# Kernel optimization log

Hardware: AMD Instinct MI355X
Metric: run time of the kernel (lower is better)

## Reference

```python
import jax, jax.numpy as jnp
import numpy as np

N = 100000
E = 1600000
D_IN = 256
D_OUT = 128
ALPHA = 0.2  # LeakyReLU negative slope


def setup_inputs() -> dict:
    key = jax.random.key(0)
    k1, k2, k3, k4, k5 = jax.random.split(key, 5)
    x = jax.random.normal(k1, (N, D_IN), dtype=jnp.float32)
    # random edges + self-loops so every destination row has >=1 incoming edge
    src = jax.random.randint(k2, (E - N,), 0, N)
    dst = jax.random.randint(k3, (E - N,), 0, N)
    loops = jnp.arange(N)
    edge = jnp.stack([jnp.concatenate([src, loops]),
                      jnp.concatenate([dst, loops])]).astype(jnp.int64)  # [2, E]
    W = jax.random.normal(k4, (D_IN, D_OUT), dtype=jnp.float32) * 0.1
    a = jax.random.normal(k5, (1, 2 * D_OUT), dtype=jnp.float32) * 0.1
    return {"x": x, "edge": edge, "W": W, "a": a}


def reference(x, edge, W, a):
    n = x.shape[0]
    d_out = W.shape[1]
    h = x @ W  # [n, d_out]
    src, dst = edge[0], edge[1]
    # a @ concat(h[src], h[dst]) decomposes into two per-node projections
    f_src = h @ a[0, :d_out]   # [n]
    f_dst = h @ a[0, d_out:]   # [n]
    tmp = f_src[src] + f_dst[dst]                      # [E]
    lrelu = jnp.where(tmp > 0, tmp, ALPHA * tmp)
    edge_e = jnp.exp(-lrelu)                           # [E]
    # spmm(A, ones) -> rowsum; spmm(A, h) -> weighted aggregation (rows = src)
    e_rowsum = jax.ops.segment_sum(edge_e, src, num_segments=n)           # [n]
    hh = jax.ops.segment_sum(edge_e[:, None] * h[dst], src, num_segments=n)  # [n, d_out]
    hh = hh / e_rowsum[:, None]
    return jax.nn.elu(hh)  # end=False -> apply ELU
```

## Files before the change

kernel.cpp:

```cpp
#include <hip/hip_runtime.h>

#define D_IN 256
#define D_OUT 128
#define ALPHA 0.2f
#define RB 64
#define RBSH 6
#define NBMAX 1600
#define CH 8192
#define CAPG 1536
#define OVFCAP 32768
#define LDA 264

typedef __attribute__((ext_vector_type(8))) short bf16x8;
typedef __attribute__((ext_vector_type(4))) float f32x4;

__device__ inline unsigned short f2bf(float f) {
    unsigned int u = __float_as_uint(f);
    return (unsigned short)((u + 0x7FFFu + ((u >> 16) & 1u)) >> 16);
}
__device__ inline float bf2f(unsigned short u) {
    return __uint_as_float(((unsigned int)u) << 16);
}

__global__ __launch_bounds__(256) void k_wt(const float* __restrict__ W,
                                            unsigned short* __restrict__ WTb) {
    const int ncol = blockIdx.x;
    const int k = threadIdx.x;
    WTb[(size_t)ncol * 256 + k] = f2bf(W[(size_t)k * 128 + ncol]);
}

__global__ __launch_bounds__(256, 4) void k_gemm(const float* __restrict__ x,
                                                 const unsigned short* __restrict__ WTb,
                                                 const float* __restrict__ a,
                                                 unsigned short* __restrict__ hb,
                                                 float* __restrict__ f_src,
                                                 float* __restrict__ f_dst, int n) {
    __shared__ unsigned short sA[64 * LDA];
    __shared__ float sFp[64][2][2];
    const int t = threadIdx.x;
    const int l = t & 63;
    const int w = t >> 6;
    const int wr = w >> 1, wc = w & 1;
    const int row0 = blockIdx.x * 64;
    const int col0 = wc * 64;
    const int lr = l & 15;
    const int g = l >> 4;
    const int lk8 = g * 8;

    {
        const int rr = t >> 5;
        const int cc = (t & 31) * 8;
        #pragma unroll
        for (int it = 0; it < 8; ++it) {
            int r = it * 8 + rr;
            int gr = row0 + r;
            float4 fa, fb;
            if (gr < n) {
                fa = *(const float4*)&x[(size_t)gr * D_IN + cc];
                fb = *(const float4*)&x[(size_t)gr * D_IN + cc + 4];
            } else {
                fa = make_float4(0.f, 0.f, 0.f, 0.f);
                fb = fa;
            }
            bf16x8 v;
            v[0] = (short)f2bf(fa.x); v[1] = (short)f2bf(fa.y);
            v[2] = (short)f2bf(fa.z); v[3] = (short)f2bf(fa.w);
            v[4] = (short)f2bf(fb.x); v[5] = (short)f2bf(fb.y);
            v[6] = (short)f2bf(fb.z); v[7] = (short)f2bf(fb.w);
            *(bf16x8*)&sA[r * LDA + cc] = v;
        }
    }
    __syncthreads();

    f32x4 acc[2][4] = {};
    const unsigned short* bp[4];
    #pragma unroll
    for (int ni = 0; ni < 4; ++ni)
        bp[ni] = WTb + (size_t)(col0 + ni * 16 + lr) * 256 + lk8;

    #pragma unroll
    for (int k0 = 0; k0 < D_IN; k0 += 32) {
        bf16x8 af[2], bfr[4];
        #pragma unroll
        for (int mi = 0; mi < 2; ++mi)
            af[mi] = *(const bf16x8*)&sA[(wr * 32 + mi * 16 + lr) * LDA + k0 + lk8];
        #pragma unroll
        for (int ni = 0; ni < 4; ++ni) bfr[ni] = *(const bf16x8*)(bp[ni] + k0);
        #pragma unroll
        for (int mi = 0; mi < 2; ++mi)
            #pragma unroll
            for (int ni = 0; ni < 4; ++ni)
                acc[mi][ni] = __builtin_amdgcn_mfma_f32_16x16x32_bf16(
                    af[mi], bfr[ni], acc[mi][ni], 0, 0, 0);
    }

    #pragma unroll
    for (int mi = 0; mi < 2; ++mi) {
        #pragma unroll
        for (int q = 0; q < 4; ++q) {
            int r = row0 + wr * 32 + mi * 16 + g * 4 + q;
            if (r < n) {
                #pragma unroll
                for (int ni = 0; ni < 4; ++ni)
                    hb[(size_t)r * D_OUT + col0 + ni * 16 + lr] =
                        f2bf(acc[mi][ni][q]);
            }
        }
    }

    float asv[4], adv[4];
    #pragma unroll
    for (int ni = 0; ni < 4; ++ni) {
        asv[ni] = a[col0 + ni * 16 + lr];
        adv[ni] = a[D_OUT + col0 + ni * 16 + lr];
    }
    #pragma unroll
    for (int mi = 0; mi < 2; ++mi) {
        #pragma unroll
        for (int q = 0; q < 4; ++q) {
            float fs = 0.f, fd = 0.f;
            #pragma unroll
            for (int ni = 0; ni < 4; ++ni) {
                float v = acc[mi][ni][q];
                fs = fmaf(v, asv[ni], fs);
                fd = fmaf(v, adv[ni], fd);
            }
            #pragma unroll
            for (int m = 1; m < 16; m <<= 1) {
                fs += __shfl_xor(fs, m);
                fd += __shfl_xor(fd, m);
            }
            if (lr == 0) {
                int rl = wr * 32 + mi * 16 + g * 4 + q;
                sFp[rl][wc][0] = fs;
                sFp[rl][wc][1] = fd;
            }
        }
    }
    __syncthreads();
    if (t < 64) {
        int r = row0 + t;
        if (r < n) {
            f_src[r] = sFp[t][0][0] + sFp[t][1][0];
            f_dst[r] = sFp[t][0][1] + sFp[t][1][1];
        }
    }
}

__global__ __launch_bounds__(256) void k_bfill(const int* __restrict__ src,
                                               const int* __restrict__ dst,
                                               int* __restrict__ gcnt,
                                               int2* __restrict__ ovf,
                                               int* __restrict__ gkeys, int E, int nb) {
    __shared__ int cnt[NBMAX];
    __shared__ int bas[NBMAX];
    const int t = threadIdx.x;
    const int e0 = blockIdx.x * CH;
    const int e1 = min(e0 + CH, E);
    for (int i = t; i < nb; i += 256) cnt[i] = 0;
    __syncthreads();
    for (int e = e0 + t; e < e1; e += 256) atomicAdd(&cnt[src[e] >> RBSH], 1);
    __syncthreads();
    for (int b = t; b < nb; b += 256) {
        int c = cnt[b];
        bas[b] = c ? atomicAdd(&gcnt[b], c) : 0;
        cnt[b] = 0;
    }
    __syncthreads();
    for (int e = e0 + t; e < e1; e += 256) {
        int s = src[e], d = dst[e];
        int b = s >> RBSH;
        int key = ((s & (RB - 1)) << 17) | d;
        int r = bas[b] + atomicAdd(&cnt[b], 1);
        if (r < CAPG) {
            gkeys[b * CAPG + r] = key;
        } else {
            int o = atomicAdd(&gcnt[nb], 1);
            if (o < OVFCAP) ovf[o] = make_int2(b, key);
        }
    }
}

__global__ __launch_bounds__(512, 8) void k_bagg(const unsigned short* __restrict__ hb,
                                                 const float* __restrict__ f_src,
                                                 const float* __restrict__ f_dst,
                                                 const int* __restrict__ gcnt,
                                                 const int2* __restrict__ ovf,
                                                 const int* __restrict__ gkeys,
                                                 float* __restrict__ out, int n, int nb) {
    __shared__ int2 sdw[CAPG];
    __shared__ int nbase[RB];
    __shared__ int ncnt[RB];
    __shared__ int ncur[RB];
    __shared__ float fsl[RB];
    __shared__ int sc[RB];
    const int t = threadIdx.x;
    const int b = blockIdx.x;
    const int s0 = b * RB;
    const int nn = min(RB, n - s0);
    const int beg = b * CAPG;
    const int stored = min(gcnt[b], CAPG);
    const int ovf_n = min(gcnt[nb], OVFCAP);

    for (int i = t; i < RB; i += 512) {
        ncnt[i] = 0;
        fsl[i] = (i < nn) ? f_src[s0 + i] : 0.f;
    }
    __syncthreads();

    for (int i = t; i < stored; i += 512)
        atomicAdd(&ncnt[gkeys[beg + i] >> 17], 1);
    __syncthreads();

    if (t < RB) sc[t] = ncnt[t];
    __syncthreads();
    for (int off = 1; off < RB; off <<= 1) {
        int v = 0;
        if (t < RB && t >= off) v = sc[t - off];
        __syncthreads();
        if (t < RB) sc[t] += v;
        __syncthreads();
    }
    if (t < RB) {
        nbase[t] = sc[t] - ncnt[t];
        ncur[t]  = sc[t] - ncnt[t];
    }
    __syncthreads();

    for (int i = t; i < stored; i += 512) {
        int k = gkeys[beg + i];
        int d = k & 0x1FFFF, ls = k >> 17;
        float tmp = fsl[ls] + f_dst[d];
        float w = __expf(-((tmp > 0.f) ? tmp : ALPHA * tmp));
        int pos = atomicAdd(&ncur[ls], 1);
        sdw[pos] = make_int2(d, __float_as_int(w));
    }
    __syncthreads();

    const int lane = t & 63, wid = t >> 6;
    const int cl = (lane & 31) * 4;
    const bool isB = lane >= 32;
    for (int ni = wid; ni < nn; ni += 8) {
        const int jb = nbase[ni];
        const int cn = ncnt[ni];
        const int halfA = (cn + 1) >> 1;
        const int halfB = cn - halfA;
        const int lim = isB ? halfB : halfA;
        const int jbh = jb + (isB ? halfA : 0);
        float a0 = 0.f, a1 = 0.f, a2 = 0.f, a3 = 0.f, rowsum = 0.f;
        #pragma unroll 4
        for (int it = 0; it < halfA; ++it) {
            bool valid = it < lim;
            int2 dw = sdw[valid ? (jbh + it) : jb];
            float w = valid ? __int_as_float(dw.y) : 0.f;
            ushort4 hv = *(const ushort4*)&hb[(size_t)dw.x * D_OUT + cl];
            rowsum += w;
            a0 = fmaf(w, bf2f(hv.x), a0);
            a1 = fmaf(w, bf2f(hv.y), a1);
            a2 = fmaf(w, bf2f(hv.z), a2);
            a3 = fmaf(w, bf2f(hv.w), a3);
        }
        if (ovf_n > 0) {
            for (int o = 0; o < ovf_n; ++o) {
                int2 ov = ovf[o];
                if (ov.x == b && (ov.y >> 17) == ni && !isB) {
                    int d = ov.y & 0x1FFFF;
                    float tmp = fsl[ni] + f_dst[d];
                    float w = __expf(-((tmp > 0.f) ? tmp : ALPHA * tmp));
                    ushort4 hv = *(const ushort4*)&hb[(size_t)d * D_OUT + cl];
                    rowsum += w;
                    a0 = fmaf(w, bf2f(hv.x), a0);
                    a1 = fmaf(w, bf2f(hv.y), a1);
                    a2 = fmaf(w, bf2f(hv.z), a2);
                    a3 = fmaf(w, bf2f(hv.w), a3);
                }
            }
        }
        rowsum += __shfl_xor(rowsum, 32);
        a0 += __shfl_xor(a0, 32);
        a1 += __shfl_xor(a1, 32);
        a2 += __shfl_xor(a2, 32);
        a3 += __shfl_xor(a3, 32);
        if (!isB) {
            float inv = 1.f / rowsum;
            a0 *= inv; a1 *= inv; a2 *= inv; a3 *= inv;
            a0 = (a0 > 0.f) ? a0 : (__expf(a0) - 1.f);
            a1 = (a1 > 0.f) ? a1 : (__expf(a1) - 1.f);
            a2 = (a2 > 0.f) ? a2 : (__expf(a2) - 1.f);
            a3 = (a3 > 0.f) ? a3 : (__expf(a3) - 1.f);
            *(float4*)&out[(size_t)(s0 + ni) * D_OUT + cl] =
                make_float4(a0, a1, a2, a3);
        }
    }
}

extern "C" void kernel_launch(void* const* d_in, const int* in_sizes, int n_in,
                              void* d_out, int out_size, void* d_ws, size_t ws_size,
                              hipStream_t stream) {
    const float* x    = (const float*)d_in[0];
    const int*   edge = (const int*)d_in[1];
    const float* W    = (const float*)d_in[2];
    const float* a    = (const float*)d_in[3];
    float* out = (float*)d_out;

    const int n = in_sizes[0] / D_IN;
    const int E = in_sizes[1] / 2;
    const int* src = edge;
    const int* dst = edge + E;
    const int nb = (n + RB - 1) / RB;

    char* p = (char*)d_ws;
    unsigned short* hb  = (unsigned short*)p; p += (size_t)n * D_OUT * sizeof(unsigned short);
    unsigned short* WTb = (unsigned short*)p; p += (size_t)D_OUT * D_IN * sizeof(unsigned short);
    float* f_src = (float*)p;  p += (size_t)n * sizeof(float);
    float* f_dst = (float*)p;  p += (size_t)n * sizeof(float);
    int*  gcnt   = (int*)p;    p += (size_t)(nb + 1) * sizeof(int);
    int2* ovf    = (int2*)p;   p += (size_t)OVFCAP * sizeof(int2);
    int*  gkeys  = (int*)p;    p += (size_t)nb * CAPG * sizeof(int);

    const int gemm_blocks = (n + 63) / 64;

    k_wt<<<D_OUT, 256, 0, stream>>>(W, WTb);
    k_gemm<<<gemm_blocks, 256, 0, stream>>>(x, WTb, a, hb, f_src, f_dst, n);

    hipMemsetAsync(gcnt, 0, (size_t)(nb + 1) * sizeof(int), stream);
    k_bfill<<<(E + CH - 1) / CH, 256, 0, stream>>>(src, dst, gcnt, ovf, gkeys, E, nb);
    k_bagg<<<nb, 512, 0, stream>>>(hb, f_src, f_dst, gcnt, ovf, gkeys, out, n, nb);
}
```

Before: 158.0 us.

## Enlarge GEMM row tile to 128 with split-K staging and XOR-swizzled LDS

The GEMM kernel now processes 128 rows per block instead of 64, so each wave computes a 64x64 tile and reuses each loaded W fragment across twice as many MFMAs. The x tile is staged in two K halves of 128 so the LDS footprint stays bounded, and an XOR swizzle replaces the old padded stride to avoid bank conflicts. The cost is more accumulator registers, an extra pair of barriers per block, and half as many blocks, which may reduce occupancy. The explicit occupancy hint in the launch bounds is also dropped.

```diff
diff --git a/kernel.cpp b/kernel.cpp
--- a/kernel.cpp
+++ b/kernel.cpp
@@ -9,7 +9,7 @@
 #define CH 8192
 #define CAPG 1536
 #define OVFCAP 32768
-#define LDA 264
+#define LKH 128
 
 typedef __attribute__((ext_vector_type(8))) short bf16x8;
 typedef __attribute__((ext_vector_type(4))) float f32x4;
@@ -29,76 +29,86 @@
     WTb[(size_t)ncol * 256 + k] = f2bf(W[(size_t)k * 128 + ncol]);
 }
 
-__global__ __launch_bounds__(256, 4) void k_gemm(const float* __restrict__ x,
-                                                 const unsigned short* __restrict__ WTb,
-                                                 const float* __restrict__ a,
-                                                 unsigned short* __restrict__ hb,
-                                                 float* __restrict__ f_src,
-                                                 float* __restrict__ f_dst, int n) {
-    __shared__ unsigned short sA[64 * LDA];
-    __shared__ float sFp[64][2][2];
+__global__ __launch_bounds__(256) void k_gemm(const float* __restrict__ x,
+                                              const unsigned short* __restrict__ WTb,
+                                              const float* __restrict__ a,
+                                              unsigned short* __restrict__ hb,
+                                              float* __restrict__ f_src,
+                                              float* __restrict__ f_dst, int n) {
+    __shared__ unsigned short sA[128 * LKH];
+    __shared__ float sFp[128][2][2];
     const int t = threadIdx.x;
     const int l = t & 63;
     const int w = t >> 6;
     const int wr = w >> 1, wc = w & 1;
-    const int row0 = blockIdx.x * 64;
+    const int row0 = blockIdx.x * 128;
     const int col0 = wc * 64;
     const int lr = l & 15;
     const int g = l >> 4;
     const int lk8 = g * 8;
 
-    {
-        const int rr = t >> 5;
-        const int cc = (t & 31) * 8;
-        #pragma unroll
-        for (int it = 0; it < 8; ++it) {
-            int r = it * 8 + rr;
-            int gr = row0 + r;
-            float4 fa, fb;
-            if (gr < n) {
-                fa = *(const float4*)&x[(size_t)gr * D_IN + cc];
-                fb = *(const float4*)&x[(size_t)gr * D_IN + cc + 4];
-            } else {
-                fa = make_float4(0.f, 0.f, 0.f, 0.f);
-                fb = fa;
-            }
-            bf16x8 v;
-            v[0] = (short)f2bf(fa.x); v[1] = (short)f2bf(fa.y);
-            v[2] = (short)f2bf(fa.z); v[3] = (short)f2bf(fa.w);
-            v[4] = (short)f2bf(fb.x); v[5] = (short)f2bf(fb.y);
-            v[6] = (short)f2bf(fb.z); v[7] = (short)f2bf(fb.w);
-            *(bf16x8*)&sA[r * LDA + cc] = v;
-        }
-    }
-    __syncthreads();
-
-    f32x4 acc[2][4] = {};
+    f32x4 acc[4][4] = {};
     const unsigned short* bp[4];
     #pragma unroll
     for (int ni = 0; ni < 4; ++ni)
         bp[ni] = WTb + (size_t)(col0 + ni * 16 + lr) * 256 + lk8;
 
     #pragma unroll
-    for (int k0 = 0; k0 < D_IN; k0 += 32) {
-        bf16x8 af[2], bfr[4];
+    for (int half = 0; half < 2; ++half) {
+        {
+            const int rr = t >> 4;
+            const int cc = (t & 15) * 8;
+            #pragma unroll
+            for (int it = 0; it < 8; ++it) {
+                int r = it * 16 + rr;
+                int gr = row0 + r;
+                float4 fa, fb;
+                if (gr < n) {
+                    const float* xp = &x[(size_t)gr * D_IN + half * LKH + cc];
+                    fa = *(const float4*)xp;
+                    fb = *(const float4*)(xp + 4);
+                } else {
+                    fa = make_float4(0.f, 0.f, 0.f, 0.f);
+                    fb = fa;
+                }
+                bf16x8 v;
+                v[0] = (short)f2bf(fa.x); v[1] = (short)f2bf(fa.y);
+                v[2] = (short)f2bf(fa.z); v[3] = (short)f2bf(fa.w);
+                v[4] = (short)f2bf(fb.x); v[5] = (short)f2bf(fb.y);
+                v[6] = (short)f2bf(fb.z); v[7] = (short)f2bf(fb.w);
+                int js = (cc >> 3) ^ ((r & 7) << 1);
+                *(bf16x8*)&sA[r * LKH + js * 8] = v;
+            }
+        }
+        __syncthreads();
+
         #pragma unroll
-        for (int mi = 0; mi < 2; ++mi)
-            af[mi] = *(const bf16x8*)&sA[(wr * 32 + mi * 16 + lr) * LDA + k0 + lk8];
-        #pragma unroll
-        for (int ni = 0; ni < 4; ++ni) bfr[ni] = *(const bf16x8*)(bp[ni] + k0);
-        #pragma unroll
-        for (int mi = 0; mi < 2; ++mi)
+        for (int k0 = 0; k0 < LKH; k0 += 32) {
+            bf16x8 af[4], bfr[4];
+            #pragma unroll
+            for (int mi = 0; mi < 4; ++mi) {
+                int row_l = wr * 64 + mi * 16 + lr;
+                int js = ((k0 >> 3) + g) ^ ((row_l & 7) << 1);
+                af[mi] = *(const bf16x8*)&sA[row_l * LKH + js * 8];
+            }
             #pragma unroll
             for (int ni = 0; ni < 4; ++ni)
-                acc[mi][ni] = __builtin_amdgcn_mfma_f32_16x16x32_bf16(
-                    af[mi], bfr[ni], acc[mi][ni], 0, 0, 0);
-    }
-
-    #pragma unroll
-    for (int mi = 0; mi < 2; ++mi) {
+                bfr[ni] = *(const bf16x8*)(bp[ni] + half * LKH + k0);
+            #pragma unroll
+            for (int mi = 0; mi < 4; ++mi)
+                #pragma unroll
+                for (int ni = 0; ni < 4; ++ni)
+                    acc[mi][ni] = __builtin_amdgcn_mfma_f32_16x16x32_bf16(
+                        af[mi], bfr[ni], acc[mi][ni], 0, 0, 0);
+        }
+        __syncthreads();
+    }
+
+    #pragma unroll
+    for (int mi = 0; mi < 4; ++mi) {
         #pragma unroll
         for (int q = 0; q < 4; ++q) {
-            int r = row0 + wr * 32 + mi * 16 + g * 4 + q;
+            int r = row0 + wr * 64 + mi * 16 + g * 4 + q;
             if (r < n) {
                 #pragma unroll
                 for (int ni = 0; ni < 4; ++ni)
@@ -115,7 +125,7 @@
         adv[ni] = a[D_OUT + col0 + ni * 16 + lr];
     }
     #pragma unroll
-    for (int mi = 0; mi < 2; ++mi) {
+    for (int mi = 0; mi < 4; ++mi) {
         #pragma unroll
         for (int q = 0; q < 4; ++q) {
             float fs = 0.f, fd = 0.f;
@@ -131,14 +141,14 @@
                 fd += __shfl_xor(fd, m);
             }
             if (lr == 0) {
-                int rl = wr * 32 + mi * 16 + g * 4 + q;
+                int rl = wr * 64 + mi * 16 + g * 4 + q;
                 sFp[rl][wc][0] = fs;
                 sFp[rl][wc][1] = fd;
             }
         }
     }
     __syncthreads();
-    if (t < 64) {
+    if (t < 128) {
         int r = row0 + t;
         if (r < n) {
             f_src[r] = sFp[t][0][0] + sFp[t][1][0];
@@ -318,7 +328,7 @@
     int2* ovf    = (int2*)p;   p += (size_t)OVFCAP * sizeof(int2);
     int*  gkeys  = (int*)p;    p += (size_t)nb * CAPG * sizeof(int);
 
-    const int gemm_blocks = (n + 63) / 64;
+    const int gemm_blocks = (n + 127) / 128;
 
     k_wt<<<D_OUT, 256, 0, stream>>>(W, WTb);
     k_gemm<<<gemm_blocks, 256, 0, stream>>>(x, WTb, a, hb, f_src, f_dst, n);
```

Result: faster. 152.2 us (-3.7%).
